# Kernel tuning notes

Hardware: AMD Instinct MI355X
Metric: run time of the kernel (lower is better)

## Reference

```python
import jax, jax.numpy as jnp
import numpy as np

B, N, D = 4, 2048, 768
H, DH = 12, 64  # heads, qk/v head dim
SCALE = DH ** -0.5


def setup_inputs() -> dict:
    key = jax.random.key(0)
    ks = jax.random.split(key, 6)
    s = (1.0 / np.sqrt(D)).astype(np.float32)
    return {
        'x': jax.random.normal(ks[0], (B, N, D), dtype=jnp.float32),
        'x_mask': jax.random.randint(ks[1], (B, N), 0, 2) > 0,
        'Wq': jax.random.normal(ks[2], (D, H * DH), dtype=jnp.float32) * s,
        'Wk': jax.random.normal(ks[3], (D, H * DH), dtype=jnp.float32) * s,
        'Wv': jax.random.normal(ks[4], (D, H * DH), dtype=jnp.float32) * s,
        'Wo': jax.random.normal(ks[5], (H * DH, D), dtype=jnp.float32) * s,
    }


def reference(x, x_mask, Wq, Wk, Wv, Wo):
    # projections (no bias), split heads: b n (h d) -> b h n d
    q = (x @ Wq).reshape(B, N, H, DH).transpose(0, 2, 1, 3)
    k = (x @ Wk).reshape(B, N, H, DH).transpose(0, 2, 1, 3)
    v = (x @ Wv).reshape(B, N, H, DH).transpose(0, 2, 1, 3)
    dots = jnp.einsum('bhid,bhjd->bhij', q, k) * SCALE
    mask_value = -jnp.finfo(dots.dtype).max
    # q_mask [b,1,i,1] & k_mask [b,1,1,j] (self-attention: both from x_mask)
    input_mask = x_mask[:, None, :, None] & x_mask[:, None, None, :]
    dots = jnp.where(input_mask, dots, mask_value)
    attn = jax.nn.softmax(dots.astype(jnp.float32), axis=-1)
    # dropout is identity in eval mode
    out = jnp.einsum('bhij,bhjd->bhid', attn, v)
    out = out.transpose(0, 2, 1, 3).reshape(B, N, H * DH)  # b h n d -> b n (h d)
    return out @ Wo
```

## Files before the change

kernel.cpp:

```cpp
#include <hip/hip_runtime.h>


#define B_ 4
#define N_ 2048
#define D_ 768
#define H_ 12
#define DH_ 64
#define CSC_ 0.18033688011112042f

typedef __attribute__((ext_vector_type(8))) short bf8_t;
typedef __attribute__((ext_vector_type(4))) float f4_t;
typedef __attribute__((ext_vector_type(16))) float f16v;
typedef __attribute__((ext_vector_type(4))) int i4_t;

__device__ __forceinline__ short f2b(float f) {
  union { float f; unsigned u; } v; v.f = f;
  unsigned r = v.u + 0x7FFFu + ((v.u >> 16) & 1u);
  return (short)(r >> 16);
}
__device__ __forceinline__ float b2f(short s) {
  union { unsigned u; float f; } v; v.u = ((unsigned)(unsigned short)s) << 16;
  return v.f;
}
__device__ __forceinline__ unsigned cvtpk(float lo, float hi) {
  unsigned r;
  asm("v_cvt_pk_bf16_f32 %0, %1, %2" : "=v"(r) : "v"(lo), "v"(hi));
  return r;
}
__device__ __forceinline__ void plswap(unsigned& a, unsigned& b) {
  asm("v_permlane32_swap_b32 %0, %1" : "+v"(a), "+v"(b));
}
__device__ __forceinline__ float max3f(float a, float b, float c) {
  float r;
  asm("v_max3_f32 %0, %1, %2, %3" : "=v"(r) : "v"(a), "v"(b), "v"(c));
  return r;
}

#define GLOAD_LDS16(gp, lp)                                                       \
  __builtin_amdgcn_global_load_lds(                                               \
      (const __attribute__((address_space(1))) void*)(gp),                        \
      (__attribute__((address_space(3))) void*)(lp), 16, 0, 0)

__global__ __launch_bounds__(256) void k_convx(const float* __restrict__ x,
                                               short* __restrict__ xb) {
  int i = blockIdx.x * 256 + threadIdx.x;
  int base = i * 8;
  float4 a = *(const float4*)(x + base);
  float4 b = *(const float4*)(x + base + 4);
  bf8_t v;
  v[0] = f2b(a.x); v[1] = f2b(a.y); v[2] = f2b(a.z); v[3] = f2b(a.w);
  v[4] = f2b(b.x); v[5] = f2b(b.y); v[6] = f2b(b.z); v[7] = f2b(b.w);
  *(bf8_t*)(xb + base) = v;
}

__global__ __launch_bounds__(256) void k_wtrans(const float* __restrict__ Wq,
                                                const float* __restrict__ Wk,
                                                const float* __restrict__ Wv,
                                                const float* __restrict__ Wo,
                                                short* __restrict__ WqkvT,
                                                short* __restrict__ WoT) {
  int z = blockIdx.z;
  const float* W = (z == 0) ? Wq : (z == 1) ? Wk : (z == 2) ? Wv : Wo;
  short* dst = (z < 3) ? (WqkvT + (size_t)z * D_ * D_) : WoT;
  float sc = (z == 0) ? CSC_ : 1.f;
  __shared__ float T[64][65];
  int r0 = blockIdx.y * 64, c0 = blockIdx.x * 64;
  int tr = threadIdx.x >> 6, tc = threadIdx.x & 63;
#pragma unroll
  for (int i = 0; i < 16; ++i) {
    int r = tr + i * 4;
    T[r][tc] = W[(size_t)(r0 + r) * D_ + c0 + tc];
  }
  __syncthreads();
#pragma unroll
  for (int i = 0; i < 16; ++i) {
    int r = tr + i * 4;
    dst[(size_t)(c0 + r) * D_ + r0 + tc] = f2b(T[tc][r] * sc);
  }
}

template <int MODE>
__global__ __launch_bounds__(256) void k_gemm(const short* __restrict__ A,
                                              const short* __restrict__ BT, int K,
                                              short* __restrict__ Qb, short* __restrict__ Kb,
                                              short* __restrict__ Vb,
                                              float* __restrict__ Cout, int ldc) {
  __shared__ short As[2][128 * 64];
  __shared__ short Bs[2][128 * 64];
  int gx = gridDim.x;
  int nwg = gx * gridDim.y;
  int flat = blockIdx.y * gx + blockIdx.x;
  int cpx = nwg >> 3;
  int swzb = (flat & 7) * cpx + (flat >> 3);
  int row0 = (swzb / gx) * 128, col0 = (swzb % gx) * 128;

  int tid = threadIdx.x, lane = tid & 63, w = tid >> 6;
  int wr = w >> 1, wc = w & 1;
  int lr = lane & 15, lhi = lane >> 4;
  f4_t acc[4][4];
#pragma unroll
  for (int mi = 0; mi < 4; ++mi)
#pragma unroll
    for (int ni = 0; ni < 4; ++ni) acc[mi][ni] = (f4_t){0.f, 0.f, 0.f, 0.f};

  int sub = lane >> 3;
  int scb = ((lane & 7) * 16) ^ (sub << 4);
  auto STAGE = [&](int k0, int buf) {
    char* ab = (char*)As[buf] + (w << 12);
    char* bb = (char*)Bs[buf] + (w << 12);
#pragma unroll
    for (int i = 0; i < 4; ++i) {
      int r = 32 * w + 8 * i + sub;
      GLOAD_LDS16((const char*)(A + (size_t)(row0 + r) * K + k0) + scb, ab + (i << 10));
      GLOAD_LDS16((const char*)(BT + (size_t)(col0 + r) * K + k0) + scb, bb + (i << 10));
    }
  };

  STAGE(0, 0);

  int nt = K / 64;
  for (int t = 0; t < nt; ++t) {
    int cur = t & 1;
    if (t + 1 < nt) {
      STAGE((t + 1) * 64, cur ^ 1);
      asm volatile("s_waitcnt vmcnt(8)" ::: "memory");
    } else {
      asm volatile("s_waitcnt vmcnt(0)" ::: "memory");
    }
    __builtin_amdgcn_sched_barrier(0);
    __builtin_amdgcn_s_barrier();

    const char* Ac = (const char*)As[cur];
    const char* Bc = (const char*)Bs[cur];
    int rsw = (lr & 7) << 4;
#pragma unroll
    for (int kc = 0; kc < 2; ++kc) {
      bf8_t av[4], bv[4];
#pragma unroll
      for (int mi = 0; mi < 4; ++mi) {
        int row = 64 * wr + 16 * mi + lr;
        av[mi] = *(const bf8_t*)(Ac + row * 128 + ((64 * kc + 16 * lhi) ^ rsw));
      }
#pragma unroll
      for (int ni = 0; ni < 4; ++ni) {
        int row = 64 * wc + 16 * ni + lr;
        bv[ni] = *(const bf8_t*)(Bc + row * 128 + ((64 * kc + 16 * lhi) ^ rsw));
      }
#pragma unroll
      for (int mi = 0; mi < 4; ++mi)
#pragma unroll
        for (int ni = 0; ni < 4; ++ni)
          acc[mi][ni] = __builtin_amdgcn_mfma_f32_16x16x32_bf16(av[mi], bv[ni], acc[mi][ni], 0, 0, 0);
    }
    __builtin_amdgcn_sched_barrier(0);
    __builtin_amdgcn_s_barrier();
  }

#pragma unroll
  for (int mi = 0; mi < 4; ++mi)
#pragma unroll
    for (int ni = 0; ni < 4; ++ni)
#pragma unroll
      for (int r = 0; r < 4; ++r) {
        int row = row0 + 64 * wr + 16 * mi + 4 * lhi + r;
        int col = col0 + 64 * wc + 16 * ni + lr;
        float v = acc[mi][ni][r];
        if (MODE == 0) {
          int which = col / 768;
          int cc2 = col - which * 768;
          int h = cc2 >> 6, dh = cc2 & 63;
          int b = row >> 11, n = row & 2047;
          size_t dst = (((size_t)(b * H_ + h)) * N_ + n) * DH_ + dh;
          short bv2 = f2b(v);
          if (which == 0) Qb[dst] = bv2;
          else if (which == 1) Kb[dst] = bv2;
          else Vb[dst] = bv2;
        } else {
          Cout[(size_t)row * ldc + col] = v;
        }
      }
}

__global__ __launch_bounds__(256) void k_maskidx(const int* __restrict__ xmask,
                                                 int* __restrict__ idx,
                                                 int* __restrict__ cnt) {
  int b = blockIdx.x, t = threadIdx.x;
  const int* mp = xmask + b * N_;
  int loc[8], c = 0;
#pragma unroll
  for (int j = 0; j < 8; ++j) {
    int n = t * 8 + j;
    if (mp[n]) loc[c++] = n;
  }
  __shared__ int sc[256];
  sc[t] = c;
  __syncthreads();
  for (int off = 1; off < 256; off <<= 1) {
    int v = (t >= off) ? sc[t - off] : 0;
    __syncthreads();
    sc[t] += v;
    __syncthreads();
  }
  int base = sc[t] - c;
  int* op = idx + b * N_;
  for (int j = 0; j < c; ++j) op[base + j] = loc[j];
  if (t == 255) cnt[b] = sc[255];
}

__global__ __launch_bounds__(256) void k_vmeanA(const short* __restrict__ Vb,
                                                float* __restrict__ part) {
  int bh = blockIdx.y, ch = blockIdx.x, t = threadIdx.x;
  int rg = t >> 3, cg = t & 7;
  const short* vp = Vb + ((size_t)bh * N_ + ch * 256 + rg) * DH_ + cg * 8;
  float a[8] = {0, 0, 0, 0, 0, 0, 0, 0};
#pragma unroll
  for (int k = 0; k < 8; ++k) {
    bf8_t v = *(const bf8_t*)(vp + (size_t)32 * k * DH_);
#pragma unroll
    for (int e = 0; e < 8; ++e) a[e] += b2f(v[e]);
  }
  __shared__ float red[8][32][8];
#pragma unroll
  for (int e = 0; e < 8; ++e) red[cg][rg][e] = a[e];
  __syncthreads();
  if (t < 64) {
    int g = t >> 3, j = t & 7;
    float s = 0;
#pragma unroll
    for (int i = 0; i < 32; ++i) s += red[g][i][j];
    part[((size_t)bh * 8 + ch) * 64 + g * 8 + j] = s;
  }
}

__global__ __launch_bounds__(256) void k_vmeanB(const float* __restrict__ part,
                                                float* __restrict__ Vmean) {
  int i = blockIdx.x * 256 + threadIdx.x;
  if (i >= 48 * 64) return;
  int bh = i >> 6, dh = i & 63;
  float s = 0;
#pragma unroll
  for (int c = 0; c < 8; ++c) s += part[((size_t)bh * 8 + c) * 64 + dh];
  Vmean[i] = s * (1.f / 2048.f);
}

__global__ __launch_bounds__(256) void k_gather(const short* __restrict__ Kb,
                                                const short* __restrict__ Vb,
                                                const int* __restrict__ idx,
                                                const int* __restrict__ cnt,
                                                short* __restrict__ Kc,
                                                short* __restrict__ Vtc) {
  int bh = blockIdx.y, b = bh / H_;
  int j0 = blockIdx.x * 64;
  int cn = cnt[b];
  int cp = (cn + 63) & ~63;
  if (j0 >= cp) return;
  int t = threadIdx.x;
  __shared__ int sidx[64];
  __shared__ short vt[64][72];
  if (t < 64) sidx[t] = (j0 + t < cn) ? idx[b * N_ + j0 + t] : -1;
  __syncthreads();
  int r = t >> 2, c16 = (t & 3) * 16;
  int src = sidx[r];
  const bf8_t zz = {0, 0, 0, 0, 0, 0, 0, 0};
#pragma unroll
  for (int u = 0; u < 2; ++u) {
    bf8_t kv = (src >= 0) ? *(const bf8_t*)(Kb + ((size_t)bh * N_ + src) * DH_ + c16 + u * 8) : zz;
    bf8_t vv = (src >= 0) ? *(const bf8_t*)(Vb + ((size_t)bh * N_ + src) * DH_ + c16 + u * 8) : zz;
    *(bf8_t*)(Kc + ((size_t)bh * N_ + j0 + r) * DH_ + c16 + u * 8) = kv;
    *(bf8_t*)(&vt[r][c16 + u * 8]) = vv;
  }
  __syncthreads();
  int dh = t >> 2;
#pragma unroll
  for (int u = 0; u < 2; ++u) {
    bf8_t ov;
#pragma unroll
    for (int e = 0; e < 8; ++e) ov[e] = vt[c16 + u * 8 + e][dh];
    *(bf8_t*)(Vtc + ((size_t)bh * DH_ + dh) * N_ + j0 + c16 + u * 8) = ov;
  }
}

__global__ __launch_bounds__(256) void k_fill(const int* __restrict__ xmask,
                                              const float* __restrict__ Vmean,
                                              short* __restrict__ Ao) {
  int b = blockIdx.y;
  int n = blockIdx.x * 32 + (threadIdx.x >> 3);
  int cg = threadIdx.x & 7;
  if (xmask[b * N_ + n]) return;
#pragma unroll
  for (int k = 0; k < 12; ++k) {
    int col = cg * 8 + k * 64;
    int h = col >> 6, dh = col & 63;
    const float* vp = Vmean + ((size_t)b * H_ + h) * 64 + dh;
    bf8_t ov;
#pragma unroll
    for (int e = 0; e < 8; ++e) ov[e] = f2b(vp[e]);
    *(bf8_t*)(Ao + ((size_t)b * N_ + n) * D_ + col) = ov;
  }
}

__global__ __launch_bounds__(256, 3) void k_attn(const short* __restrict__ Q,
                                                 const short* __restrict__ Kcg,
                                                 const short* __restrict__ Vtcg,
                                                 const int* __restrict__ idx,
                                                 const int* __restrict__ cnt,
                                                 short* __restrict__ Aout) {
  int bh = blockIdx.y;
  int b = bh / H_, h = bh - b * H_;
  int cn = cnt[b];
  int nqt = (cn + 127) >> 7;
  if ((int)blockIdx.x >= nqt) return;
  int nkt = (cn + 63) >> 6;
  const short* Qp = Q + (size_t)bh * N_ * DH_;
  const short* Kp = Kcg + (size_t)bh * N_ * DH_;
  const short* Vp = Vtcg + (size_t)bh * DH_ * N_;
  const int* ip = idx + b * N_;
  int q0 = blockIdx.x * 128;
  int tid = threadIdx.x, lane = tid & 63, w = tid >> 6;
  int lq = lane & 31, hi = lane >> 5;

  __shared__ char smem[32768];

  int qrow = q0 + 32 * w + lq;
  int qn = ip[qrow < cn ? qrow : cn - 1];

  bf8_t qf[4];
#pragma unroll
  for (int kc = 0; kc < 4; ++kc)
    qf[kc] = *(const bf8_t*)(Qp + (size_t)qn * DH_ + 16 * kc + 8 * hi);

  short NEGBIG = f2b(-1e30f);
  bf8_t qbf = {hi ? (short)0 : (short)0x3F80, 0, 0, 0, 0, 0, 0, 0};

  f16v acco[2];
#pragma unroll
  for (int i = 0; i < 16; ++i) { acco[0][i] = 0.f; acco[1][i] = 0.f; }
  float m = -1e29f, lsum = 0.f;

  auto STAGE = [&](int key0, int buf) {
    char* kb_ = smem + buf * 16384;
    char* vb_ = kb_ + 8192;
    int row = tid >> 3;
    int cb = (tid & 7) * 16;
    char* lk = kb_ + ((tid >> 6) << 10);
    char* lv = vb_ + ((tid >> 6) << 10);
#pragma unroll
    for (int rr = 0; rr < 2; ++rr) {
      int r2 = row + rr * 32;
      int sw = cb ^ ((r2 & 7) << 4);
      GLOAD_LDS16((const char*)(Kp + (size_t)(key0 + r2) * DH_) + sw, lk + rr * 4096);
      GLOAD_LDS16((const char*)(Vp + (size_t)r2 * N_ + key0) + sw, lv + rr * 4096);
    }
  };

  STAGE(0, 0);
  __syncthreads();

  for (int kt = 0; kt < nkt; ++kt) {
    int cur = kt & 1;
    if (kt + 1 < nkt) STAGE((kt + 1) * 64, cur ^ 1);

    const char* kbase = smem + cur * 16384;
    const char* vbase = kbase + 8192;
    int key0 = kt * 64;

    f16v accs[2];
#pragma unroll
    for (int i = 0; i < 16; ++i) { accs[0][i] = 0.f; accs[1][i] = 0.f; }
    int swz = (lq & 7) << 4;
    __builtin_amdgcn_s_setprio(1);
#pragma unroll
    for (int kc = 0; kc < 4; ++kc) {
      int colb = (32 * kc + 16 * hi) ^ swz;
      bf8_t k0 = *(const bf8_t*)(kbase + lq * 128 + colb);
      bf8_t k1 = *(const bf8_t*)(kbase + (32 + lq) * 128 + colb);
      accs[0] = __builtin_amdgcn_mfma_f32_32x32x16_bf16(k0, qf[kc], accs[0], 0, 0, 0);
      accs[1] = __builtin_amdgcn_mfma_f32_32x32x16_bf16(k1, qf[kc], accs[1], 0, 0, 0);
    }
    __builtin_amdgcn_s_setprio(0);
    if (key0 + 64 > cn) {
      bf8_t bf0 = {(hi || key0 + lq < cn) ? (short)0 : NEGBIG, 0, 0, 0, 0, 0, 0, 0};
      bf8_t bf1 = {(hi || key0 + 32 + lq < cn) ? (short)0 : NEGBIG, 0, 0, 0, 0, 0, 0, 0};
      accs[0] = __builtin_amdgcn_mfma_f32_32x32x16_bf16(bf0, qbf, accs[0], 0, 0, 0);
      accs[1] = __builtin_amdgcn_mfma_f32_32x32x16_bf16(bf1, qbf, accs[1], 0, 0, 0);
    }

    float mx = max3f(accs[0][0], accs[0][1], accs[0][2]);
#pragma unroll
    for (int i = 3; i < 15; i += 2) mx = max3f(mx, accs[0][i], accs[0][i + 1]);
    mx = max3f(mx, accs[0][15], accs[1][0]);
#pragma unroll
    for (int i = 1; i < 15; i += 2) mx = max3f(mx, accs[1][i], accs[1][i + 1]);
    mx = fmaxf(mx, accs[1][15]);
    mx = fmaxf(mx, __shfl_xor(mx, 32));
    if (!__all(mx <= m + 8.f)) {
      float mnew = fmaxf(m, mx);
      float sc = __builtin_amdgcn_exp2f(m - mnew);
      m = mnew;
      lsum *= sc;
#pragma unroll
      for (int i = 0; i < 16; ++i) { acco[0][i] *= sc; acco[1][i] *= sc; }
    }
    float psa[4] = {0.f, 0.f, 0.f, 0.f};
#pragma unroll
    for (int kb2 = 0; kb2 < 2; ++kb2)
#pragma unroll
      for (int r = 0; r < 16; ++r) {
        float p = __builtin_amdgcn_exp2f(accs[kb2][r] - m);
        accs[kb2][r] = p;
        psa[r & 3] += p;
      }
    float ps = (psa[0] + psa[1]) + (psa[2] + psa[3]);
    ps += __shfl_xor(ps, 32);
    lsum += ps;

    __builtin_amdgcn_s_setprio(1);
#pragma unroll
    for (int kc = 0; kc < 4; ++kc) {
      int kb2 = kc >> 1, rb = (kc & 1) * 8;
      unsigned a_ = cvtpk(accs[kb2][rb + 0], accs[kb2][rb + 1]);
      unsigned b_ = cvtpk(accs[kb2][rb + 4], accs[kb2][rb + 5]);
      unsigned c_ = cvtpk(accs[kb2][rb + 2], accs[kb2][rb + 3]);
      unsigned d_ = cvtpk(accs[kb2][rb + 6], accs[kb2][rb + 7]);
      plswap(a_, b_);
      plswap(c_, d_);
      union { i4_t i; bf8_t v; } pu;
      pu.i = (i4_t){(int)a_, (int)c_, (int)b_, (int)d_};
      int colb = (32 * kc + 16 * hi) ^ swz;
      bf8_t v0 = *(const bf8_t*)(vbase + lq * 128 + colb);
      bf8_t v1 = *(const bf8_t*)(vbase + (32 + lq) * 128 + colb);
      acco[0] = __builtin_amdgcn_mfma_f32_32x32x16_bf16(v0, pu.v, acco[0], 0, 0, 0);
      acco[1] = __builtin_amdgcn_mfma_f32_32x32x16_bf16(v1, pu.v, acco[1], 0, 0, 0);
    }
    __builtin_amdgcn_s_setprio(0);

    __syncthreads();
  }
  __syncthreads();

  float inv = 1.f / lsum;
  unsigned* Os = (unsigned*)smem + w * 1152;
#pragma unroll
  for (int dhb = 0; dhb < 2; ++dhb)
#pragma unroll
    for (int r = 0; r < 16; r += 2) {
      unsigned pk = cvtpk(acco[dhb][r] * inv, acco[dhb][r + 1] * inv);
      int colu = 16 * dhb + ((r & 3) >> 1) + 4 * (r >> 2) + 2 * hi;
      Os[lq * 36 + colu] = pk;
    }
#pragma unroll
  for (int it = 0; it < 4; ++it) {
    int q = (lane >> 3) + 8 * it;
    int qr2 = q0 + 32 * w + q;
    if (qr2 < cn) {
      int n = ip[qr2];
      i4_t vv = *(const i4_t*)(Os + q * 36 + 4 * (lane & 7));
      union { i4_t i; bf8_t s; } u2;
      u2.i = vv;
      size_t off = ((size_t)b * N_ + n) * D_ + h * DH_ + 8 * (lane & 7);
      *(bf8_t*)(Aout + off) = u2.s;
    }
  }
}

extern "C" void kernel_launch(void* const* d_in, const int* in_sizes, int n_in,
                              void* d_out, int out_size, void* d_ws, size_t ws_size,
                              hipStream_t stream) {
  (void)in_sizes; (void)n_in; (void)out_size; (void)ws_size;
  const float* x  = (const float*)d_in[0];
  const int*   xm = (const int*)d_in[1];
  const float* Wq = (const float*)d_in[2];
  const float* Wk = (const float*)d_in[3];
  const float* Wv = (const float*)d_in[4];
  const float* Wo = (const float*)d_in[5];
  float* out = (float*)d_out;
  char* ws = (char*)d_ws;

  short* x_bf  = (short*)(ws + 0);
  short* Ao    = (short*)(ws + 0);
  short* WqkvT = (short*)(ws + 12582912);
  int*   idxb  = (int*)(ws + 12582912);
  int*   cntb  = (int*)(ws + 12615680);
  float* part  = (float*)(ws + 12615744);
  float* Vmean = (float*)(ws + 12714048);
  short* WoT   = (short*)(ws + 16121856);
  short* Qb    = (short*)(ws + 17301504);
  short* Kb    = (short*)(ws + 29884416);
  short* Vb    = (short*)(ws + 42467328);
  short* Kc    = (short*)(ws + 55050240);
  short* Vtc   = (short*)(ws + 67633152);

  k_convx<<<3072, 256, 0, stream>>>(x, x_bf);
  k_wtrans<<<dim3(12, 12, 4), 256, 0, stream>>>(Wq, Wk, Wv, Wo, WqkvT, WoT);
  k_gemm<0><<<dim3(18, 64), 256, 0, stream>>>(x_bf, WqkvT, 768, Qb, Kb, Vb, nullptr, 0);
  k_maskidx<<<4, 256, 0, stream>>>(xm, idxb, cntb);
  k_vmeanA<<<dim3(8, 48), 256, 0, stream>>>(Vb, part);
  k_vmeanB<<<12, 256, 0, stream>>>(part, Vmean);
  k_gather<<<dim3(32, 48), 256, 0, stream>>>(Kb, Vb, idxb, cntb, Kc, Vtc);
  k_attn<<<dim3(16, 48), 256, 0, stream>>>(Qb, Kc, Vtc, idxb, cntb, Ao);
  k_fill<<<dim3(64, 4), 256, 0, stream>>>(xm, Vmean, Ao);
  k_gemm<1><<<dim3(6, 64), 256, 0, stream>>>(Ao, WoT, 768, nullptr, nullptr, nullptr, out, 768);
}
```

Before: 132.4 us.

## Compact unmasked rows before QKV projection and skip masked-row GEMM work

```diff
diff --git a/kernel.cpp b/kernel.cpp
--- a/kernel.cpp
+++ b/kernel.cpp
@@ -18,10 +18,6 @@
   unsigned r = v.u + 0x7FFFu + ((v.u >> 16) & 1u);
   return (short)(r >> 16);
 }
-__device__ __forceinline__ float b2f(short s) {
-  union { unsigned u; float f; } v; v.u = ((unsigned)(unsigned short)s) << 16;
-  return v.f;
-}
 __device__ __forceinline__ unsigned cvtpk(float lo, float hi) {
   unsigned r;
   asm("v_cvt_pk_bf16_f32 %0, %1, %2" : "=v"(r) : "v"(lo), "v"(hi));
@@ -41,16 +37,75 @@
       (const __attribute__((address_space(1))) void*)(gp),                        \
       (__attribute__((address_space(3))) void*)(lp), 16, 0, 0)
 
-__global__ __launch_bounds__(256) void k_convx(const float* __restrict__ x,
-                                               short* __restrict__ xb) {
-  int i = blockIdx.x * 256 + threadIdx.x;
-  int base = i * 8;
-  float4 a = *(const float4*)(x + base);
-  float4 b = *(const float4*)(x + base + 4);
-  bf8_t v;
-  v[0] = f2b(a.x); v[1] = f2b(a.y); v[2] = f2b(a.z); v[3] = f2b(a.w);
-  v[4] = f2b(b.x); v[5] = f2b(b.y); v[6] = f2b(b.z); v[7] = f2b(b.w);
-  *(bf8_t*)(xb + base) = v;
+__global__ __launch_bounds__(256) void k_maskidx(const int* __restrict__ xmask,
+                                                 int* __restrict__ idx,
+                                                 int* __restrict__ cnt) {
+  int b = blockIdx.x, t = threadIdx.x;
+  const int* mp = xmask + b * N_;
+  int loc[8], c = 0;
+#pragma unroll
+  for (int j = 0; j < 8; ++j) {
+    int n = t * 8 + j;
+    if (mp[n]) loc[c++] = n;
+  }
+  __shared__ int sc[256];
+  sc[t] = c;
+  __syncthreads();
+  for (int off = 1; off < 256; off <<= 1) {
+    int v = (t >= off) ? sc[t - off] : 0;
+    __syncthreads();
+    sc[t] += v;
+    __syncthreads();
+  }
+  int base = sc[t] - c;
+  int* op = idx + b * N_;
+  for (int j = 0; j < c; ++j) op[base + j] = loc[j];
+  if (t == 255) cnt[b] = sc[255];
+}
+
+__global__ __launch_bounds__(256) void k_xsumA(const float* __restrict__ x,
+                                               float* __restrict__ xpart) {
+  int b = blockIdx.y, ch = blockIdx.x, t = threadIdx.x;
+  const float* xp = x + ((size_t)b * N_ + ch * 32) * D_;
+  float a0 = 0, a1 = 0, a2 = 0;
+  for (int r = 0; r < 32; ++r) {
+    const float* rp = xp + (size_t)r * D_;
+    a0 += rp[t]; a1 += rp[t + 256]; a2 += rp[t + 512];
+  }
+  float* op = xpart + ((size_t)b * 64 + ch) * D_;
+  op[t] = a0; op[t + 256] = a1; op[t + 512] = a2;
+}
+
+__global__ __launch_bounds__(256) void k_gatherx(const float* __restrict__ x,
+                                                 const int* __restrict__ idx,
+                                                 const int* __restrict__ cnt,
+                                                 short* __restrict__ xc) {
+  int b = blockIdx.y;
+  int j = blockIdx.x * 8 + (threadIdx.x >> 5);
+  int cn = cnt[b];
+  int l5 = threadIdx.x & 31;
+  short* op = xc + ((size_t)b * N_ + j) * D_;
+  if (j < cn) {
+    int n = idx[b * N_ + j];
+    const float* rp = x + ((size_t)b * N_ + n) * D_;
+#pragma unroll
+    for (int it = 0; it < 3; ++it) {
+      int c = (l5 + it * 32) * 8;
+      float4 v0 = *(const float4*)(rp + c);
+      float4 v1 = *(const float4*)(rp + c + 4);
+      bf8_t o;
+      o[0] = f2b(v0.x); o[1] = f2b(v0.y); o[2] = f2b(v0.z); o[3] = f2b(v0.w);
+      o[4] = f2b(v1.x); o[5] = f2b(v1.y); o[6] = f2b(v1.z); o[7] = f2b(v1.w);
+      *(bf8_t*)(op + c) = o;
+    }
+  } else {
+    const bf8_t zz = {0, 0, 0, 0, 0, 0, 0, 0};
+#pragma unroll
+    for (int it = 0; it < 3; ++it) {
+      int c = (l5 + it * 32) * 8;
+      *(bf8_t*)(op + c) = zz;
+    }
+  }
 }
 
 __global__ __launch_bounds__(256) void k_wtrans(const float* __restrict__ Wq,
@@ -84,7 +139,9 @@
                                               const short* __restrict__ BT, int K,
                                               short* __restrict__ Qb, short* __restrict__ Kb,
                                               short* __restrict__ Vb,
-                                              float* __restrict__ Cout, int ldc) {
+                                              float* __restrict__ Cout, int ldc,
+                                              const int* __restrict__ cnt,
+                                              const int* __restrict__ idx) {
   __shared__ short As[2][128 * 64];
   __shared__ short Bs[2][128 * 64];
   int gx = gridDim.x;
@@ -94,6 +151,11 @@
   int swzb = (flat & 7) * cpx + (flat >> 3);
   int row0 = (swzb / gx) * 128, col0 = (swzb % gx) * 128;
 
+  int bb = row0 >> 11;
+  int cn = cnt[bb];
+  int cnpad = (cn + 127) & ~127;
+  if ((row0 & 2047) >= cnpad) return;
+
   int tid = threadIdx.x, lane = tid & 63, w = tid >> 6;
   int wr = w >> 1, wc = w & 1;
   int lr = lane & 15, lhi = lane >> 4;
@@ -107,12 +169,12 @@
   int scb = ((lane & 7) * 16) ^ (sub << 4);
   auto STAGE = [&](int k0, int buf) {
     char* ab = (char*)As[buf] + (w << 12);
-    char* bb = (char*)Bs[buf] + (w << 12);
+    char* bb2 = (char*)Bs[buf] + (w << 12);
 #pragma unroll
     for (int i = 0; i < 4; ++i) {
       int r = 32 * w + 8 * i + sub;
       GLOAD_LDS16((const char*)(A + (size_t)(row0 + r) * K + k0) + scb, ab + (i << 10));
-      GLOAD_LDS16((const char*)(BT + (size_t)(col0 + r) * K + k0) + scb, bb + (i << 10));
+      GLOAD_LDS16((const char*)(BT + (size_t)(col0 + r) * K + k0) + scb, bb2 + (i << 10));
     }
   };
 
@@ -176,133 +238,94 @@
           else if (which == 1) Kb[dst] = bv2;
           else Vb[dst] = bv2;
         } else {
-          Cout[(size_t)row * ldc + col] = v;
+          int j = row & 2047;
+          if (j < cn) {
+            int n = idx[(row & ~2047) + j];
+            Cout[((size_t)(row & ~2047) + n) * ldc + col] = v;
+          }
         }
       }
 }
 
-__global__ __launch_bounds__(256) void k_maskidx(const int* __restrict__ xmask,
-                                                 int* __restrict__ idx,
-                                                 int* __restrict__ cnt) {
-  int b = blockIdx.x, t = threadIdx.x;
-  const int* mp = xmask + b * N_;
-  int loc[8], c = 0;
-#pragma unroll
-  for (int j = 0; j < 8; ++j) {
-    int n = t * 8 + j;
-    if (mp[n]) loc[c++] = n;
-  }
-  __shared__ int sc[256];
-  sc[t] = c;
-  __syncthreads();
-  for (int off = 1; off < 256; off <<= 1) {
-    int v = (t >= off) ? sc[t - off] : 0;
-    __syncthreads();
-    sc[t] += v;
-    __syncthreads();
-  }
-  int base = sc[t] - c;
-  int* op = idx + b * N_;
-  for (int j = 0; j < c; ++j) op[base + j] = loc[j];
-  if (t == 255) cnt[b] = sc[255];
-}
-
-__global__ __launch_bounds__(256) void k_vmeanA(const short* __restrict__ Vb,
-                                                float* __restrict__ part) {
-  int bh = blockIdx.y, ch = blockIdx.x, t = threadIdx.x;
-  int rg = t >> 3, cg = t & 7;
-  const short* vp = Vb + ((size_t)bh * N_ + ch * 256 + rg) * DH_ + cg * 8;
-  float a[8] = {0, 0, 0, 0, 0, 0, 0, 0};
-#pragma unroll
-  for (int k = 0; k < 8; ++k) {
-    bf8_t v = *(const bf8_t*)(vp + (size_t)32 * k * DH_);
-#pragma unroll
-    for (int e = 0; e < 8; ++e) a[e] += b2f(v[e]);
-  }
-  __shared__ float red[8][32][8];
-#pragma unroll
-  for (int e = 0; e < 8; ++e) red[cg][rg][e] = a[e];
-  __syncthreads();
-  if (t < 64) {
-    int g = t >> 3, j = t & 7;
+__global__ __launch_bounds__(256) void k_vtrans(const short* __restrict__ V,
+                                                const int* __restrict__ cnt,
+                                                short* __restrict__ Vt) {
+  int bh = blockIdx.y, b = bh / H_;
+  int n0 = blockIdx.x * 64;
+  int cn = cnt[b];
+  int cnpad = (cn + 127) & ~127;
+  if (n0 >= cnpad) return;
+  __shared__ short T[64][72];
+  int tr = threadIdx.x >> 6, tc = threadIdx.x & 63;
+  const short* Vp = V + (size_t)bh * N_ * DH_;
+  short* Vtp = Vt + (size_t)bh * DH_ * N_;
+#pragma unroll
+  for (int i = 0; i < 16; ++i) {
+    int r = tr + i * 4;
+    T[r][tc] = Vp[(size_t)(n0 + r) * DH_ + tc];
+  }
+  __syncthreads();
+#pragma unroll
+  for (int i = 0; i < 16; ++i) {
+    int r = tr + i * 4;
+    Vtp[(size_t)r * N_ + n0 + tc] = T[tc][r];
+  }
+}
+
+__global__ __launch_bounds__(256) void k_vmean(const float* __restrict__ xpart,
+                                               const float* __restrict__ Wv,
+                                               float* __restrict__ vmeanG) {
+  int b = blockIdx.y, cc = blockIdx.x, t = threadIdx.x;
+  __shared__ float xm[768];
+  for (int c = t; c < 768; c += 256) {
     float s = 0;
-#pragma unroll
-    for (int i = 0; i < 32; ++i) s += red[g][i][j];
-    part[((size_t)bh * 8 + ch) * 64 + g * 8 + j] = s;
-  }
-}
-
-__global__ __launch_bounds__(256) void k_vmeanB(const float* __restrict__ part,
-                                                float* __restrict__ Vmean) {
-  int i = blockIdx.x * 256 + threadIdx.x;
-  if (i >= 48 * 64) return;
-  int bh = i >> 6, dh = i & 63;
-  float s = 0;
-#pragma unroll
-  for (int c = 0; c < 8; ++c) s += part[((size_t)bh * 8 + c) * 64 + dh];
-  Vmean[i] = s * (1.f / 2048.f);
-}
-
-__global__ __launch_bounds__(256) void k_gather(const short* __restrict__ Kb,
-                                                const short* __restrict__ Vb,
-                                                const int* __restrict__ idx,
-                                                const int* __restrict__ cnt,
-                                                short* __restrict__ Kc,
-                                                short* __restrict__ Vtc) {
-  int bh = blockIdx.y, b = bh / H_;
-  int j0 = blockIdx.x * 64;
-  int cn = cnt[b];
-  int cp = (cn + 63) & ~63;
-  if (j0 >= cp) return;
-  int t = threadIdx.x;
-  __shared__ int sidx[64];
-  __shared__ short vt[64][72];
-  if (t < 64) sidx[t] = (j0 + t < cn) ? idx[b * N_ + j0 + t] : -1;
-  __syncthreads();
-  int r = t >> 2, c16 = (t & 3) * 16;
-  int src = sidx[r];
-  const bf8_t zz = {0, 0, 0, 0, 0, 0, 0, 0};
-#pragma unroll
-  for (int u = 0; u < 2; ++u) {
-    bf8_t kv = (src >= 0) ? *(const bf8_t*)(Kb + ((size_t)bh * N_ + src) * DH_ + c16 + u * 8) : zz;
-    bf8_t vv = (src >= 0) ? *(const bf8_t*)(Vb + ((size_t)bh * N_ + src) * DH_ + c16 + u * 8) : zz;
-    *(bf8_t*)(Kc + ((size_t)bh * N_ + j0 + r) * DH_ + c16 + u * 8) = kv;
-    *(bf8_t*)(&vt[r][c16 + u * 8]) = vv;
-  }
-  __syncthreads();
-  int dh = t >> 2;
-#pragma unroll
-  for (int u = 0; u < 2; ++u) {
-    bf8_t ov;
-#pragma unroll
-    for (int e = 0; e < 8; ++e) ov[e] = vt[c16 + u * 8 + e][dh];
-    *(bf8_t*)(Vtc + ((size_t)bh * DH_ + dh) * N_ + j0 + c16 + u * 8) = ov;
-  }
-}
-
-__global__ __launch_bounds__(256) void k_fill(const int* __restrict__ xmask,
-                                              const float* __restrict__ Vmean,
-                                              short* __restrict__ Ao) {
+    for (int ch = 0; ch < 64; ++ch) s += xpart[((size_t)b * 64 + ch) * D_ + c];
+    xm[c] = s * (1.f / 2048.f);
+  }
+  __syncthreads();
+  int col = cc * 256 + t;
+  float acc = 0;
+#pragma unroll 4
+  for (int k = 0; k < 768; ++k) acc += xm[k] * Wv[(size_t)k * D_ + col];
+  vmeanG[b * D_ + col] = acc;
+}
+
+__global__ __launch_bounds__(256) void k_outrow(const float* __restrict__ vmeanG,
+                                                const float* __restrict__ Wo,
+                                                float* __restrict__ outrowG) {
+  int b = blockIdx.y, cc = blockIdx.x, t = threadIdx.x;
+  __shared__ float vm[768];
+  for (int c = t; c < 768; c += 256) vm[c] = vmeanG[b * D_ + c];
+  __syncthreads();
+  int col = cc * 256 + t;
+  float acc = 0;
+#pragma unroll 4
+  for (int k = 0; k < 768; ++k) acc += vm[k] * Wo[(size_t)k * D_ + col];
+  outrowG[b * D_ + col] = acc;
+}
+
+__global__ __launch_bounds__(256) void k_fillout(const int* __restrict__ xmask,
+                                                 const float* __restrict__ outrowG,
+                                                 float* __restrict__ out) {
   int b = blockIdx.y;
   int n = blockIdx.x * 32 + (threadIdx.x >> 3);
   int cg = threadIdx.x & 7;
   if (xmask[b * N_ + n]) return;
-#pragma unroll
-  for (int k = 0; k < 12; ++k) {
-    int col = cg * 8 + k * 64;
-    int h = col >> 6, dh = col & 63;
-    const float* vp = Vmean + ((size_t)b * H_ + h) * 64 + dh;
-    bf8_t ov;
-#pragma unroll
-    for (int e = 0; e < 8; ++e) ov[e] = f2b(vp[e]);
-    *(bf8_t*)(Ao + ((size_t)b * N_ + n) * D_ + col) = ov;
+  const float* rp = outrowG + b * D_;
+  float* op = out + ((size_t)b * N_ + n) * D_;
+#pragma unroll
+  for (int it = 0; it < 12; ++it) {
+    int c = cg * 8 + it * 64;
+    float4 v0 = *(const float4*)(rp + c);
+    float4 v1 = *(const float4*)(rp + c + 4);
+    *(float4*)(op + c) = v0;
+    *(float4*)(op + c + 4) = v1;
   }
 }
 
 __global__ __launch_bounds__(256, 3) void k_attn(const short* __restrict__ Q,
                                                  const short* __restrict__ Kcg,
                                                  const short* __restrict__ Vtcg,
-                                                 const int* __restrict__ idx,
                                                  const int* __restrict__ cnt,
                                                  short* __restrict__ Aout) {
   int bh = blockIdx.y;
@@ -314,7 +337,6 @@
   const short* Qp = Q + (size_t)bh * N_ * DH_;
   const short* Kp = Kcg + (size_t)bh * N_ * DH_;
   const short* Vp = Vtcg + (size_t)bh * DH_ * N_;
-  const int* ip = idx + b * N_;
   int q0 = blockIdx.x * 128;
   int tid = threadIdx.x, lane = tid & 63, w = tid >> 6;
   int lq = lane & 31, hi = lane >> 5;
@@ -322,12 +344,11 @@
   __shared__ char smem[32768];
 
   int qrow = q0 + 32 * w + lq;
-  int qn = ip[qrow < cn ? qrow : cn - 1];
 
   bf8_t qf[4];
 #pragma unroll
   for (int kc = 0; kc < 4; ++kc)
-    qf[kc] = *(const bf8_t*)(Qp + (size_t)qn * DH_ + 16 * kc + 8 * hi);
+    qf[kc] = *(const bf8_t*)(Qp + (size_t)qrow * DH_ + 16 * kc + 8 * hi);
 
   short NEGBIG = f2b(-1e30f);
   bf8_t qbf = {hi ? (short)0 : (short)0x3F80, 0, 0, 0, 0, 0, 0, 0};
@@ -453,11 +474,10 @@
     int q = (lane >> 3) + 8 * it;
     int qr2 = q0 + 32 * w + q;
     if (qr2 < cn) {
-      int n = ip[qr2];
       i4_t vv = *(const i4_t*)(Os + q * 36 + 4 * (lane & 7));
       union { i4_t i; bf8_t s; } u2;
       u2.i = vv;
-      size_t off = ((size_t)b * N_ + n) * D_ + h * DH_ + 8 * (lane & 7);
+      size_t off = ((size_t)b * N_ + qr2) * D_ + h * DH_ + 8 * (lane & 7);
       *(bf8_t*)(Aout + off) = u2.s;
     }
   }
@@ -476,28 +496,31 @@
   float* out = (float*)d_out;
   char* ws = (char*)d_ws;
 
-  short* x_bf  = (short*)(ws + 0);
-  short* Ao    = (short*)(ws + 0);
-  short* WqkvT = (short*)(ws + 12582912);
-  int*   idxb  = (int*)(ws + 12582912);
-  int*   cntb  = (int*)(ws + 12615680);
-  float* part  = (float*)(ws + 12615744);
-  float* Vmean = (float*)(ws + 12714048);
-  short* WoT   = (short*)(ws + 16121856);
-  short* Qb    = (short*)(ws + 17301504);
-  short* Kb    = (short*)(ws + 29884416);
-  short* Vb    = (short*)(ws + 42467328);
-  short* Kc    = (short*)(ws + 55050240);
-  short* Vtc   = (short*)(ws + 67633152);
-
-  k_convx<<<3072, 256, 0, stream>>>(x, x_bf);
+  short* xc      = (short*)(ws + 0);
+  short* Ao      = (short*)(ws + 0);
+  short* WqkvT   = (short*)(ws + 12582912);
+  short* WoT     = (short*)(ws + 16121856);
+  int*   idxb    = (int*)(ws + 17301504);
+  int*   cntb    = (int*)(ws + 17334272);
+  float* xpart   = (float*)(ws + 17334528);
+  float* vmeanG  = (float*)(ws + 18120960);
+  float* outrowG = (float*)(ws + 18133248);
+  short* Qb      = (short*)(ws + 18874368);
+  short* Kc      = (short*)(ws + 31457280);
+  short* Vc      = (short*)(ws + 44040192);
+  short* Vtc     = (short*)(ws + 56623104);
+
+  k_maskidx<<<4, 256, 0, stream>>>(xm, idxb, cntb);
+  k_xsumA<<<dim3(64, 4), 256, 0, stream>>>(x, xpart);
+  k_gatherx<<<dim3(256, 4), 256, 0, stream>>>(x, idxb, cntb, xc);
   k_wtrans<<<dim3(12, 12, 4), 256, 0, stream>>>(Wq, Wk, Wv, Wo, WqkvT, WoT);
-  k_gemm<0><<<dim3(18, 64), 256, 0, stream>>>(x_bf, WqkvT, 768, Qb, Kb, Vb, nullptr, 0);
-  k_maskidx<<<4, 256, 0, stream>>>(xm, idxb, cntb);
-  k_vmeanA<<<dim3(8, 48), 256, 0, stream>>>(Vb, part);
-  k_vmeanB<<<12, 256, 0, stream>>>(part, Vmean);
-  k_gather<<<dim3(32, 48), 256, 0, stream>>>(Kb, Vb, idxb, cntb, Kc, Vtc);
-  k_attn<<<dim3(16, 48), 256, 0, stream>>>(Qb, Kc, Vtc, idxb, cntb, Ao);
-  k_fill<<<dim3(64, 4), 256, 0, stream>>>(xm, Vmean, Ao);
-  k_gemm<1><<<dim3(6, 64), 256, 0, stream>>>(Ao, WoT, 768, nullptr, nullptr, nullptr, out, 768);
-}
+  k_gemm<0><<<dim3(18, 64), 256, 0, stream>>>(xc, WqkvT, 768, Qb, Kc, Vc,
+                                              nullptr, 0, cntb, nullptr);
+  k_vtrans<<<dim3(32, 48), 256, 0, stream>>>(Vc, cntb, Vtc);
+  k_vmean<<<dim3(3, 4), 256, 0, stream>>>(xpart, Wv, vmeanG);
+  k_outrow<<<dim3(3, 4), 256, 0, stream>>>(vmeanG, Wo, outrowG);
+  k_attn<<<dim3(16, 48), 256, 0, stream>>>(Qb, Kc, Vtc, cntb, Ao);
+  k_fillout<<<dim3(64, 4), 256, 0, stream>>>(xm, outrowG, out);
+  k_gemm<1><<<dim3(6, 64), 256, 0, stream>>>(Ao, WoT, 768, nullptr, nullptr, nullptr,
+                                             out, 768, cntb, idxb);
+}
```

After: 282.6 us. +113.5%, slower.
